# Kernel tuning notes

Hardware: AMD Instinct MI355X
Metric: run time of the kernel (lower is better)

The kernel has to match this reference:

```python
import jax, jax.numpy as jnp
import numpy as np

H, DH = 8, 64            # heads, dim_head (inner_dim = 512)
W_DOT = 1.0              # mask_cond['para']['w_dot']
TOTAL_STEP = 50


def split_heads(x):
    # 'b n (h d) -> (b h) n d'
    b, n, _ = x.shape
    return x.reshape(b, n, H, DH).transpose(0, 2, 1, 3).reshape(b * H, n, DH)


def merge_heads(x):
    # '(b h) n d -> b n (h d)'
    bh, n, d = x.shape
    b = bh // H
    return x.reshape(b, H, n, d).transpose(0, 2, 1, 3).reshape(b, n, H * d)


def setup_inputs() -> dict:
    key = jax.random.key(0)
    ks = jax.random.split(key, 10)
    B, N, DQ, DC, L, C = 1, 4096, 320, 768, 77, 4
    INNER = H * DH
    w = lambda i, shape: jax.random.normal(ks[i], shape, jnp.float32) * 0.02
    return {
        "x": jax.random.normal(ks[0], (2 * B, N, DQ), jnp.float32),
        "uc_context": jax.random.normal(ks[1], (B, L, DC), jnp.float32),
        "ck": jax.random.normal(ks[2], (C, B, L, DC), jnp.float32),
        "cv": jax.random.normal(ks[3], (C, B, L, DC), jnp.float32),
        "attn_extra": jax.random.uniform(ks[4], (H, N, L), jnp.float32),
        "Wq": w(5, (DQ, INNER)),
        "Wk": w(6, (DC, INNER)),
        "Wv": w(7, (DC, INNER)),
        "Wo": w(8, (INNER, DQ)),
        "bo": jnp.zeros((DQ,), jnp.float32),
        "t": 10,
    }


def reference(x, uc_context, ck, cv, attn_extra, Wq, Wk, Wv, Wo, bo, t):
    scale = DH ** (-0.5)
    # schedule()['linear'][TOTAL_STEP - t - 1] == t / 50 * 4.6
    weight = (t / TOTAL_STEP) * 4.6

    B = uc_context.shape[0]
    true_bs = B * H

    q = split_heads(x @ Wq)                          # [(2B)H, N, d]
    k_uc = split_heads(uc_context @ Wk)              # [BH, L, d]
    v_uc = split_heads(uc_context @ Wv)
    k_c = jax.vmap(lambda c: split_heads(c @ Wk))(ck)  # [C, BH, L, d]
    v_c = jax.vmap(lambda c: split_heads(c @ Wv))(cv)

    q_uc, q_c = q[:true_bs], q[true_bs:]
    sim_uc = jnp.einsum('bid,bjd->bij', q_uc, k_uc) * scale     # [BH, N, L]
    sim_c = jnp.einsum('bid,cbjd->cbij', q_c, k_c) * scale      # [C, BH, N, L]

    # region-dependent additive soft mask on the first conditional branch,
    # weighted by w_dot * schedule_weight * max(sim_c[0])
    wmask = W_DOT * weight * sim_c[0].max()
    sim_c = sim_c.at[0].add(wmask * attn_extra)     # attn_extra [H, N, L] broadcasts (B=1)

    attn_uc = jax.nn.softmax(sim_uc, axis=-1)
    attn_c = jax.nn.softmax(sim_c, axis=-1)

    out_uc = jnp.einsum('bij,bjd->bid', attn_uc, v_uc)
    out_c = jnp.einsum('cbij,cbjd->bid', attn_c, v_c) / v_c.shape[0]

    out = jnp.concatenate([out_uc, out_c], axis=0)  # [2BH, N, d]
    out = merge_heads(out)                          # [2B, N, inner]
    return out @ Wo + bo                            # to_out (dropout=0 -> identity)
```

## Files before the change

kernel.cpp:

```cpp
#include <hip/hip_runtime.h>


typedef __attribute__((ext_vector_type(8))) short          bf16x8;
typedef __attribute__((ext_vector_type(4))) float          f32x4;
typedef __attribute__((ext_vector_type(8))) unsigned short u16x8;

#define OFF_XB   0ull
#define OFF_CTXB 5242880ull
#define OFF_WQT  6307840ull
#define OFF_WKT  6635520ull
#define OFF_WVT  7421952ull
#define OFF_WOT  8208384ull
#define OFF_Q    8536064ull
#define OFF_K    16924672ull
#define OFF_VT   17318912ull
#define OFF_ATT  18138112ull
#define OFF_MAX  26526720ull

__device__ __forceinline__ unsigned short bf_cvt(float f) {
  unsigned u = __float_as_uint(f);
  unsigned r = u + 0x7FFFu + ((u >> 16) & 1u);
  return (unsigned short)(r >> 16);
}
__device__ __forceinline__ unsigned enc_f(float f) {
  int b = __float_as_int(f);
  return (b >= 0) ? ((unsigned)b | 0x80000000u) : ~(unsigned)b;
}
__device__ __forceinline__ float dec_f(unsigned u) {
  unsigned b = (u & 0x80000000u) ? (u ^ 0x80000000u) : ~u;
  return __int_as_float((int)b);
}

__global__ __launch_bounds__(256) void k_convert(const float* __restrict__ x,
                                                 const float* __restrict__ uc,
                                                 const float* __restrict__ ck,
                                                 const float* __restrict__ cv,
                                                 unsigned short* __restrict__ xb,
                                                 unsigned short* __restrict__ ctxb,
                                                 unsigned* __restrict__ maxslot) {
  size_t idx = (size_t)blockIdx.x * 256 + threadIdx.x;
  if (idx == 0) *maxslot = 0u;
  if (idx < 655360) {
    float4 v = reinterpret_cast<const float4*>(x)[idx];
    ushort4 o = {bf_cvt(v.x), bf_cvt(v.y), bf_cvt(v.z), bf_cvt(v.w)};
    reinterpret_cast<ushort4*>(xb)[idx] = o;
  } else {
    size_t r = idx - 655360;
    if (r < 133056) {
      const float4* s = (r < 14784) ? (reinterpret_cast<const float4*>(uc) + r)
                      : (r < 73920) ? (reinterpret_cast<const float4*>(ck) + (r - 14784))
                                    : (reinterpret_cast<const float4*>(cv) + (r - 73920));
      float4 v = *s;
      ushort4 o = {bf_cvt(v.x), bf_cvt(v.y), bf_cvt(v.z), bf_cvt(v.w)};
      reinterpret_cast<ushort4*>(ctxb)[r] = o;
    }
  }
}

__global__ __launch_bounds__(256) void k_tw(const float* __restrict__ Wq, const float* __restrict__ Wk,
                                            const float* __restrict__ Wv, const float* __restrict__ Wo,
                                            unsigned short* __restrict__ WqT, unsigned short* __restrict__ WkT,
                                            unsigned short* __restrict__ WvT, unsigned short* __restrict__ WoT) {
  __shared__ float T[32][33];
  int z = blockIdx.z;
  const float* src; unsigned short* dst; int R, C;
  if (z == 0)      { src = Wq; dst = WqT; R = 320; C = 512; }
  else if (z == 1) { src = Wk; dst = WkT; R = 768; C = 512; }
  else if (z == 2) { src = Wv; dst = WvT; R = 768; C = 512; }
  else             { src = Wo; dst = WoT; R = 512; C = 320; }
  int c0 = blockIdx.x * 32, r0 = blockIdx.y * 32;
  if (c0 >= C || r0 >= R) return;
  int t = threadIdx.x;
  {
    int r = t >> 3, c4 = (t & 7) * 4;
    float4 v = *reinterpret_cast<const float4*>(src + (size_t)(r0 + r) * C + c0 + c4);
    T[r][c4] = v.x; T[r][c4 + 1] = v.y; T[r][c4 + 2] = v.z; T[r][c4 + 3] = v.w;
  }
  __syncthreads();
  {
    int c = t >> 3, r4 = (t & 7) * 4;
    ushort4 o = {bf_cvt(T[r4][c]), bf_cvt(T[r4 + 1][c]), bf_cvt(T[r4 + 2][c]), bf_cvt(T[r4 + 3][c])};
    *reinterpret_cast<ushort4*>(dst + (size_t)(c0 + c) * R + r0 + r4) = o;
  }
}

__global__ __launch_bounds__(256) void k_gemm_q(const unsigned short* __restrict__ xb,
                                                const unsigned short* __restrict__ WqT,
                                                unsigned short* __restrict__ q) {
  __shared__ unsigned short As[128 * 40];
  __shared__ unsigned short Bs[128 * 40];
  int tid = threadIdx.x, lane = tid & 63, w = tid >> 6;
  int wr = w >> 1, wc = w & 1, l15 = lane & 15, qd = lane >> 4;
  int mb = blockIdx.x * 128, nb = blockIdx.y * 128;
  f32x4 acc[4][4] = {};
  for (int k0 = 0; k0 < 320; k0 += 32) {
    for (int u = tid; u < 512; u += 256) {
      int r = u >> 2, c8 = (u & 3) * 8;
      *reinterpret_cast<u16x8*>(&As[r * 40 + c8]) =
          *reinterpret_cast<const u16x8*>(&xb[(size_t)(mb + r) * 320 + k0 + c8]);
    }
    for (int u = tid; u < 512; u += 256) {
      int r = u >> 2, c8 = (u & 3) * 8;
      *reinterpret_cast<u16x8*>(&Bs[r * 40 + c8]) =
          *reinterpret_cast<const u16x8*>(&WqT[(size_t)(nb + r) * 320 + k0 + c8]);
    }
    __syncthreads();
    bf16x8 a[4], b[4];
#pragma unroll
    for (int mi = 0; mi < 4; ++mi)
      a[mi] = *reinterpret_cast<const bf16x8*>(&As[(wr * 64 + mi * 16 + l15) * 40 + qd * 8]);
#pragma unroll
    for (int ni = 0; ni < 4; ++ni)
      b[ni] = *reinterpret_cast<const bf16x8*>(&Bs[(wc * 64 + ni * 16 + l15) * 40 + qd * 8]);
#pragma unroll
    for (int mi = 0; mi < 4; ++mi)
#pragma unroll
      for (int ni = 0; ni < 4; ++ni)
        acc[mi][ni] = __builtin_amdgcn_mfma_f32_16x16x32_bf16(a[mi], b[ni], acc[mi][ni], 0, 0, 0);
    __syncthreads();
  }
#pragma unroll
  for (int mi = 0; mi < 4; ++mi)
#pragma unroll
    for (int ni = 0; ni < 4; ++ni)
#pragma unroll
      for (int r = 0; r < 4; ++r) {
        int m = mb + wr * 64 + mi * 16 + qd * 4 + r;
        int n = nb + wc * 64 + ni * 16 + l15;
        int b_ = m >> 12, i = m & 4095, h = n >> 6, d = n & 63;
        q[((size_t)((b_ * 8 + h) * 4096 + i)) * 64 + d] = bf_cvt(acc[mi][ni][r]);
      }
}

__global__ __launch_bounds__(256) void k_gemm_ctx(const unsigned short* __restrict__ ctxb,
                                                  const unsigned short* __restrict__ WkT,
                                                  const unsigned short* __restrict__ WvT,
                                                  unsigned short* __restrict__ kb,
                                                  unsigned short* __restrict__ vt) {
  __shared__ unsigned short As[80 * 40];
  __shared__ unsigned short Bs[64 * 40];
  int tid = threadIdx.x, lane = tid & 63, w = tid >> 6;
  int l15 = lane & 15, qd = lane >> 4;
  int nb = blockIdx.x * 64;
  int g = blockIdx.y;
  int kv = g >= 5, cidx = g % 5;
  int src = kv ? (cidx == 0 ? 0 : 4 + cidx) : (cidx == 0 ? 0 : cidx);
  const unsigned short* WT = kv ? WvT : WkT;
  f32x4 acc[5] = {};
  for (int k0 = 0; k0 < 768; k0 += 32) {
    for (int u = tid; u < 320; u += 256) {
      int r = u >> 2, c8 = (u & 3) * 8;
      u16x8 v = {0, 0, 0, 0, 0, 0, 0, 0};
      if (r < 77) v = *reinterpret_cast<const u16x8*>(&ctxb[(size_t)(src * 77 + r) * 768 + k0 + c8]);
      *reinterpret_cast<u16x8*>(&As[r * 40 + c8]) = v;
    }
    for (int u = tid; u < 256; u += 256) {
      int r = u >> 2, c8 = (u & 3) * 8;
      *reinterpret_cast<u16x8*>(&Bs[r * 40 + c8]) =
          *reinterpret_cast<const u16x8*>(&WT[(size_t)(nb + r) * 768 + k0 + c8]);
    }
    __syncthreads();
    bf16x8 b = *reinterpret_cast<const bf16x8*>(&Bs[(w * 16 + l15) * 40 + qd * 8]);
#pragma unroll
    for (int mi = 0; mi < 5; ++mi) {
      bf16x8 a = *reinterpret_cast<const bf16x8*>(&As[(mi * 16 + l15) * 40 + qd * 8]);
      acc[mi] = __builtin_amdgcn_mfma_f32_16x16x32_bf16(a, b, acc[mi], 0, 0, 0);
    }
    __syncthreads();
  }
#pragma unroll
  for (int mi = 0; mi < 5; ++mi)
#pragma unroll
    for (int r = 0; r < 4; ++r) {
      int j = mi * 16 + qd * 4 + r;
      if (j >= 77) continue;
      int n = nb + w * 16 + l15;
      int h = n >> 6, d = n & 63;
      unsigned short val = bf_cvt(acc[mi][r]);
      if (!kv) kb[((size_t)(cidx * 8 + h) * 77 + j) * 64 + d] = val;
      else     vt[((size_t)(cidx * 8 + h) * 64 + d) * 80 + j] = val;
    }
}

__global__ __launch_bounds__(256) void k_max(const unsigned short* __restrict__ q,
                                             const unsigned short* __restrict__ kb,
                                             unsigned* __restrict__ maxslot) {
  __shared__ unsigned short Ks[80 * 72];
  __shared__ float red[4];
  int tid = threadIdx.x, lane = tid & 63, w = tid >> 6;
  int l15 = lane & 15, qd = lane >> 4;
  int rowbase = blockIdx.x * 128, h = blockIdx.y;
  size_t kbase = (size_t)(1 * 8 + h) * 77 * 64;
  for (int u = tid; u < 640; u += 256) {
    int r = u >> 3, c8 = (u & 7) * 8;
    u16x8 v = {0, 0, 0, 0, 0, 0, 0, 0};
    if (r < 77) v = *reinterpret_cast<const u16x8*>(&kb[kbase + (size_t)r * 64 + c8]);
    *reinterpret_cast<u16x8*>(&Ks[r * 72 + c8]) = v;
  }
  __syncthreads();
  bf16x8 aq[2][2];
#pragma unroll
  for (int mi = 0; mi < 2; ++mi)
#pragma unroll
    for (int ks = 0; ks < 2; ++ks) {
      int row = rowbase + w * 32 + mi * 16 + l15;
      aq[mi][ks] = *reinterpret_cast<const bf16x8*>(&q[((size_t)(8 + h) * 4096 + row) * 64 + qd * 8 + ks * 32]);
    }
  f32x4 acc[2][5] = {};
#pragma unroll
  for (int jf = 0; jf < 5; ++jf)
#pragma unroll
    for (int ks = 0; ks < 2; ++ks) {
      bf16x8 b = *reinterpret_cast<const bf16x8*>(&Ks[(jf * 16 + l15) * 72 + qd * 8 + ks * 32]);
#pragma unroll
      for (int mi = 0; mi < 2; ++mi)
        acc[mi][jf] = __builtin_amdgcn_mfma_f32_16x16x32_bf16(aq[mi][ks], b, acc[mi][jf], 0, 0, 0);
    }
  float lmax = -3.4e38f;
#pragma unroll
  for (int jf = 0; jf < 5; ++jf) {
    int j = jf * 16 + l15;
    if (j < 77) {
#pragma unroll
      for (int mi = 0; mi < 2; ++mi)
#pragma unroll
        for (int r = 0; r < 4; ++r) lmax = fmaxf(lmax, acc[mi][jf][r] * 0.125f);
    }
  }
  for (int m = 1; m < 64; m <<= 1) lmax = fmaxf(lmax, __shfl_xor(lmax, m, 64));
  if (lane == 0) red[w] = lmax;
  __syncthreads();
  if (tid == 0) {
    float m4 = fmaxf(fmaxf(red[0], red[1]), fmaxf(red[2], red[3]));
    atomicMax(maxslot, enc_f(m4));
  }
}

__global__ __launch_bounds__(256) void k_attn(const unsigned short* __restrict__ q,
                                              const unsigned short* __restrict__ kb,
                                              const unsigned short* __restrict__ vt,
                                              const float* __restrict__ extra,
                                              const int* __restrict__ tptr,
                                              const unsigned* __restrict__ maxslot,
                                              unsigned short* __restrict__ att) {
  __shared__ unsigned short Ks[80 * 72];
  __shared__ unsigned short VT[64 * 104];
  __shared__ unsigned short Ps[64 * 104];
  int tid = threadIdx.x, lane = tid & 63, w = tid >> 6;
  int l15 = lane & 15, qd = lane >> 4;
  int rowbase = blockIdx.x * 64, h = blockIdx.y, part = blockIdx.z;
  int bh = part ? 8 + h : h;
  for (int u = tid; u < 1024; u += 256) {
    int d = u >> 4, j = 80 + (u & 15);
    VT[d * 104 + j] = 0;
    Ps[d * 104 + j] = 0;
  }
  int myrow = rowbase + w * 16 + l15;
  bf16x8 aq[2];
  aq[0] = *reinterpret_cast<const bf16x8*>(&q[((size_t)bh * 4096 + myrow) * 64 + qd * 8]);
  aq[1] = *reinterpret_cast<const bf16x8*>(&q[((size_t)bh * 4096 + myrow) * 64 + qd * 8 + 32]);
  float weight = ((float)(*tptr)) * (4.6f / 50.0f);
  float wmask = weight * dec_f(*maxslot);
  int grow = rowbase + w * 16 + qd * 4;
  f32x4 oacc[4] = {};
  int nctx = part ? 4 : 1;
  for (int ci = 0; ci < nctx; ++ci) {
    int slot = part ? 1 + ci : 0;
    __syncthreads();
    size_t kbase = (size_t)(slot * 8 + h) * 77 * 64;
    size_t vbase = (size_t)(slot * 8 + h) * 64 * 80;
    for (int u = tid; u < 640; u += 256) {
      int r = u >> 3, c8 = (u & 7) * 8;
      u16x8 v = {0, 0, 0, 0, 0, 0, 0, 0};
      if (r < 77) v = *reinterpret_cast<const u16x8*>(&kb[kbase + (size_t)r * 64 + c8]);
      *reinterpret_cast<u16x8*>(&Ks[r * 72 + c8]) = v;
    }
    for (int u = tid; u < 640; u += 256) {
      int d = u / 10, c8 = (u % 10) * 8;
      *reinterpret_cast<u16x8*>(&VT[d * 104 + c8]) =
          *reinterpret_cast<const u16x8*>(&vt[vbase + (size_t)d * 80 + c8]);
    }
    __syncthreads();
    f32x4 sim[5];
#pragma unroll
    for (int jf = 0; jf < 5; ++jf) {
      bf16x8 b0 = *reinterpret_cast<const bf16x8*>(&Ks[(jf * 16 + l15) * 72 + qd * 8]);
      bf16x8 b1 = *reinterpret_cast<const bf16x8*>(&Ks[(jf * 16 + l15) * 72 + qd * 8 + 32]);
      f32x4 s = {};
      s = __builtin_amdgcn_mfma_f32_16x16x32_bf16(aq[0], b0, s, 0, 0, 0);
      s = __builtin_amdgcn_mfma_f32_16x16x32_bf16(aq[1], b1, s, 0, 0, 0);
      sim[jf] = s;
    }
    bool isc0 = (part == 1) && (ci == 0);
    float rowsum[4] = {0.f, 0.f, 0.f, 0.f};
    float e[5][4];
#pragma unroll
    for (int jf = 0; jf < 5; ++jf) {
      int j = jf * 16 + l15;
#pragma unroll
      for (int r = 0; r < 4; ++r) {
        float val = sim[jf][r] * 0.125f;
        float ev = 0.f;
        if (j < 77) {
          if (isc0) val += wmask * extra[((size_t)h * 4096 + grow + r) * 77 + j];
          ev = __expf(val);
        }
        e[jf][r] = ev;
        rowsum[r] += ev;
      }
    }
#pragma unroll
    for (int r = 0; r < 4; ++r) {
      float s = rowsum[r];
      s += __shfl_xor(s, 1, 64); s += __shfl_xor(s, 2, 64);
      s += __shfl_xor(s, 4, 64); s += __shfl_xor(s, 8, 64);
      rowsum[r] = s;
    }
#pragma unroll
    for (int jf = 0; jf < 5; ++jf) {
      int j = jf * 16 + l15;
#pragma unroll
      for (int r = 0; r < 4; ++r) Ps[(w * 16 + qd * 4 + r) * 104 + j] = bf_cvt(e[jf][r]);
    }
    bf16x8 pa[3];
#pragma unroll
    for (int ks = 0; ks < 3; ++ks)
      pa[ks] = *reinterpret_cast<const bf16x8*>(&Ps[(w * 16 + l15) * 104 + qd * 8 + ks * 32]);
#pragma unroll
    for (int nf = 0; nf < 4; ++nf) {
      f32x4 o = {};
#pragma unroll
      for (int ks = 0; ks < 3; ++ks) {
        bf16x8 bv = *reinterpret_cast<const bf16x8*>(&VT[(nf * 16 + l15) * 104 + qd * 8 + ks * 32]);
        o = __builtin_amdgcn_mfma_f32_16x16x32_bf16(pa[ks], bv, o, 0, 0, 0);
      }
      if (part == 0) {
#pragma unroll
        for (int r = 0; r < 4; ++r)
          att[((size_t)(grow + r)) * 512 + h * 64 + nf * 16 + l15] = bf_cvt(o[r] / rowsum[r]);
      } else {
#pragma unroll
        for (int r = 0; r < 4; ++r) oacc[nf][r] += o[r] / rowsum[r];
      }
    }
  }
  if (part == 1) {
#pragma unroll
    for (int nf = 0; nf < 4; ++nf)
#pragma unroll
      for (int r = 0; r < 4; ++r)
        att[((size_t)(4096 + grow + r)) * 512 + h * 64 + nf * 16 + l15] = bf_cvt(oacc[nf][r] * 0.25f);
  }
}

__global__ __launch_bounds__(256) void k_gemm_out(const unsigned short* __restrict__ att,
                                                  const unsigned short* __restrict__ WoT,
                                                  const float* __restrict__ bo,
                                                  float* __restrict__ out) {
  __shared__ unsigned short As[128 * 40];
  __shared__ unsigned short Bs[64 * 40];
  int tid = threadIdx.x, lane = tid & 63, w = tid >> 6;
  int l15 = lane & 15, qd = lane >> 4;
  int mb = blockIdx.x * 128, nb = blockIdx.y * 64;
  f32x4 acc[2][4] = {};
  for (int k0 = 0; k0 < 512; k0 += 32) {
    for (int u = tid; u < 512; u += 256) {
      int r = u >> 2, c8 = (u & 3) * 8;
      *reinterpret_cast<u16x8*>(&As[r * 40 + c8]) =
          *reinterpret_cast<const u16x8*>(&att[(size_t)(mb + r) * 512 + k0 + c8]);
    }
    for (int u = tid; u < 256; u += 256) {
      int r = u >> 2, c8 = (u & 3) * 8;
      *reinterpret_cast<u16x8*>(&Bs[r * 40 + c8]) =
          *reinterpret_cast<const u16x8*>(&WoT[(size_t)(nb + r) * 512 + k0 + c8]);
    }
    __syncthreads();
    bf16x8 a[2], b[4];
#pragma unroll
    for (int mi = 0; mi < 2; ++mi)
      a[mi] = *reinterpret_cast<const bf16x8*>(&As[(w * 32 + mi * 16 + l15) * 40 + qd * 8]);
#pragma unroll
    for (int nf = 0; nf < 4; ++nf)
      b[nf] = *reinterpret_cast<const bf16x8*>(&Bs[(nf * 16 + l15) * 40 + qd * 8]);
#pragma unroll
    for (int mi = 0; mi < 2; ++mi)
#pragma unroll
      for (int nf = 0; nf < 4; ++nf)
        acc[mi][nf] = __builtin_amdgcn_mfma_f32_16x16x32_bf16(a[mi], b[nf], acc[mi][nf], 0, 0, 0);
    __syncthreads();
  }
#pragma unroll
  for (int mi = 0; mi < 2; ++mi)
#pragma unroll
    for (int nf = 0; nf < 4; ++nf) {
      int n = nb + nf * 16 + l15;
      float bias = bo[n];
#pragma unroll
      for (int r = 0; r < 4; ++r) {
        int m = mb + w * 32 + mi * 16 + qd * 4 + r;
        out[(size_t)m * 320 + n] = acc[mi][nf][r] + bias;
      }
    }
}

extern "C" void kernel_launch(void* const* d_in, const int* in_sizes, int n_in,
                              void* d_out, int out_size, void* d_ws, size_t ws_size,
                              hipStream_t stream) {
  (void)in_sizes; (void)n_in; (void)out_size; (void)ws_size;
  const float* x  = (const float*)d_in[0];
  const float* uc = (const float*)d_in[1];
  const float* ck = (const float*)d_in[2];
  const float* cv = (const float*)d_in[3];
  const float* ex = (const float*)d_in[4];
  const float* Wq = (const float*)d_in[5];
  const float* Wk = (const float*)d_in[6];
  const float* Wv = (const float*)d_in[7];
  const float* Wo = (const float*)d_in[8];
  const float* bo = (const float*)d_in[9];
  const int*   tp = (const int*)d_in[10];

  char* base = (char*)d_ws;
  unsigned short* xb   = (unsigned short*)(base + OFF_XB);
  unsigned short* ctxb = (unsigned short*)(base + OFF_CTXB);
  unsigned short* WqT  = (unsigned short*)(base + OFF_WQT);
  unsigned short* WkT  = (unsigned short*)(base + OFF_WKT);
  unsigned short* WvT  = (unsigned short*)(base + OFF_WVT);
  unsigned short* WoT  = (unsigned short*)(base + OFF_WOT);
  unsigned short* qb   = (unsigned short*)(base + OFF_Q);
  unsigned short* kb   = (unsigned short*)(base + OFF_K);
  unsigned short* vt   = (unsigned short*)(base + OFF_VT);
  unsigned short* att  = (unsigned short*)(base + OFF_ATT);
  unsigned* maxslot    = (unsigned*)(base + OFF_MAX);

  k_convert<<<3080, 256, 0, stream>>>(x, uc, ck, cv, xb, ctxb, maxslot);
  k_tw<<<dim3(16, 24, 4), 256, 0, stream>>>(Wq, Wk, Wv, Wo, WqT, WkT, WvT, WoT);
  k_gemm_q<<<dim3(64, 4), 256, 0, stream>>>(xb, WqT, qb);
  k_gemm_ctx<<<dim3(8, 10), 256, 0, stream>>>(ctxb, WkT, WvT, kb, vt);
  k_max<<<dim3(32, 8), 256, 0, stream>>>(qb, kb, maxslot);
  k_attn<<<dim3(64, 8, 2), 256, 0, stream>>>(qb, kb, vt, ex, tp, maxslot, att);
  k_gemm_out<<<dim3(64, 5), 256, 0, stream>>>(att, WoT, bo, (float*)d_out);
}
```

Measured before the change: 176.8 us.

## Merge all stages into one persistent cooperative kernel with grid-wide syncs

Replaces the seven separate launches with a single persistent kernel that walks through phases (conversion/transpose, projections, max, attention, output GEMM) and separates them with grid-wide synchronisation. A multi-launch fallback is kept. The per-context attention outputs are now written to separate buffers and averaged while the output GEMM loads its A tile. The Wo tile is loaded with direct global-to-LDS loads and an XOR swizzle. The aim is to remove launch overhead and inter-kernel gaps, at the cost of grid-sync latency, a fixed tile schedule and extra memory traffic for the per-context buffers.

```diff
diff --git a/kernel.cpp b/kernel.cpp
--- a/kernel.cpp
+++ b/kernel.cpp
@@ -1,27 +1,44 @@
 #include <hip/hip_runtime.h>
+#include <hip/hip_cooperative_groups.h>
+
+namespace cg = cooperative_groups;
 
 
 typedef __attribute__((ext_vector_type(8))) short          bf16x8;
 typedef __attribute__((ext_vector_type(4))) float          f32x4;
 typedef __attribute__((ext_vector_type(8))) unsigned short u16x8;
 
-#define OFF_XB   0ull
-#define OFF_CTXB 5242880ull
-#define OFF_WQT  6307840ull
-#define OFF_WKT  6635520ull
-#define OFF_WVT  7421952ull
-#define OFF_WOT  8208384ull
-#define OFF_Q    8536064ull
-#define OFF_K    16924672ull
-#define OFF_VT   17318912ull
-#define OFF_ATT  18138112ull
-#define OFF_MAX  26526720ull
+#define OFF_XB    0ull
+#define OFF_CTXB  5242880ull
+#define OFF_WQT   6307328ull
+#define OFF_WKT   6635008ull
+#define OFF_WVT   7421440ull
+#define OFF_WOT   8207872ull
+#define OFF_QB    8535552ull
+#define OFF_KB    16924160ull
+#define OFF_VTB   17333760ull
+#define OFF_ATT0  18152960ull
+#define OFF_ATTC  22347264ull
+#define OFF_MAX   39124480ull
+
+#define SMEM_BYTES 38400
+
+struct Params {
+  const float *x, *uc, *ck, *cv, *ex, *Wq, *Wk, *Wv, *Wo, *bo;
+  const int* tp;
+  unsigned short *xb, *ctxb, *WqT, *WkT, *WvT, *WoT, *qb, *kb, *vtb, *att0, *attc;
+  unsigned* maxslot;
+  float* out;
+};
 
 __device__ __forceinline__ unsigned short bf_cvt(float f) {
   unsigned u = __float_as_uint(f);
   unsigned r = u + 0x7FFFu + ((u >> 16) & 1u);
   return (unsigned short)(r >> 16);
 }
+__device__ __forceinline__ float bf2f(unsigned short u) {
+  return __uint_as_float(((unsigned)u) << 16);
+}
 __device__ __forceinline__ unsigned enc_f(float f) {
   int b = __float_as_int(f);
   return (b >= 0) ? ((unsigned)b | 0x80000000u) : ~(unsigned)b;
@@ -30,413 +47,406 @@
   unsigned b = (u & 0x80000000u) ? (u ^ 0x80000000u) : ~u;
   return __int_as_float((int)b);
 }
-
-__global__ __launch_bounds__(256) void k_convert(const float* __restrict__ x,
-                                                 const float* __restrict__ uc,
-                                                 const float* __restrict__ ck,
-                                                 const float* __restrict__ cv,
-                                                 unsigned short* __restrict__ xb,
-                                                 unsigned short* __restrict__ ctxb,
-                                                 unsigned* __restrict__ maxslot) {
-  size_t idx = (size_t)blockIdx.x * 256 + threadIdx.x;
-  if (idx == 0) *maxslot = 0u;
-  if (idx < 655360) {
-    float4 v = reinterpret_cast<const float4*>(x)[idx];
-    ushort4 o = {bf_cvt(v.x), bf_cvt(v.y), bf_cvt(v.z), bf_cvt(v.w)};
-    reinterpret_cast<ushort4*>(xb)[idx] = o;
-  } else {
-    size_t r = idx - 655360;
-    if (r < 133056) {
-      const float4* s = (r < 14784) ? (reinterpret_cast<const float4*>(uc) + r)
-                      : (r < 73920) ? (reinterpret_cast<const float4*>(ck) + (r - 14784))
-                                    : (reinterpret_cast<const float4*>(cv) + (r - 73920));
-      float4 v = *s;
-      ushort4 o = {bf_cvt(v.x), bf_cvt(v.y), bf_cvt(v.z), bf_cvt(v.w)};
-      reinterpret_cast<ushort4*>(ctxb)[r] = o;
-    }
-  }
-}
-
-__global__ __launch_bounds__(256) void k_tw(const float* __restrict__ Wq, const float* __restrict__ Wk,
-                                            const float* __restrict__ Wv, const float* __restrict__ Wo,
-                                            unsigned short* __restrict__ WqT, unsigned short* __restrict__ WkT,
-                                            unsigned short* __restrict__ WvT, unsigned short* __restrict__ WoT) {
-  __shared__ float T[32][33];
-  int z = blockIdx.z;
-  const float* src; unsigned short* dst; int R, C;
-  if (z == 0)      { src = Wq; dst = WqT; R = 320; C = 512; }
-  else if (z == 1) { src = Wk; dst = WkT; R = 768; C = 512; }
-  else if (z == 2) { src = Wv; dst = WvT; R = 768; C = 512; }
-  else             { src = Wo; dst = WoT; R = 512; C = 320; }
-  int c0 = blockIdx.x * 32, r0 = blockIdx.y * 32;
-  if (c0 >= C || r0 >= R) return;
-  int t = threadIdx.x;
-  {
-    int r = t >> 3, c4 = (t & 7) * 4;
-    float4 v = *reinterpret_cast<const float4*>(src + (size_t)(r0 + r) * C + c0 + c4);
-    T[r][c4] = v.x; T[r][c4 + 1] = v.y; T[r][c4 + 2] = v.z; T[r][c4 + 3] = v.w;
-  }
-  __syncthreads();
-  {
-    int c = t >> 3, r4 = (t & 7) * 4;
-    ushort4 o = {bf_cvt(T[r4][c]), bf_cvt(T[r4 + 1][c]), bf_cvt(T[r4 + 2][c]), bf_cvt(T[r4 + 3][c])};
-    *reinterpret_cast<ushort4*>(dst + (size_t)(c0 + c) * R + r0 + r4) = o;
-  }
-}
-
-__global__ __launch_bounds__(256) void k_gemm_q(const unsigned short* __restrict__ xb,
-                                                const unsigned short* __restrict__ WqT,
-                                                unsigned short* __restrict__ q) {
-  __shared__ unsigned short As[128 * 40];
-  __shared__ unsigned short Bs[128 * 40];
-  int tid = threadIdx.x, lane = tid & 63, w = tid >> 6;
-  int wr = w >> 1, wc = w & 1, l15 = lane & 15, qd = lane >> 4;
-  int mb = blockIdx.x * 128, nb = blockIdx.y * 128;
-  f32x4 acc[4][4] = {};
-  for (int k0 = 0; k0 < 320; k0 += 32) {
-    for (int u = tid; u < 512; u += 256) {
-      int r = u >> 2, c8 = (u & 3) * 8;
-      *reinterpret_cast<u16x8*>(&As[r * 40 + c8]) =
-          *reinterpret_cast<const u16x8*>(&xb[(size_t)(mb + r) * 320 + k0 + c8]);
-    }
-    for (int u = tid; u < 512; u += 256) {
-      int r = u >> 2, c8 = (u & 3) * 8;
-      *reinterpret_cast<u16x8*>(&Bs[r * 40 + c8]) =
-          *reinterpret_cast<const u16x8*>(&WqT[(size_t)(nb + r) * 320 + k0 + c8]);
-    }
-    __syncthreads();
-    bf16x8 a[4], b[4];
-#pragma unroll
-    for (int mi = 0; mi < 4; ++mi)
-      a[mi] = *reinterpret_cast<const bf16x8*>(&As[(wr * 64 + mi * 16 + l15) * 40 + qd * 8]);
-#pragma unroll
-    for (int ni = 0; ni < 4; ++ni)
-      b[ni] = *reinterpret_cast<const bf16x8*>(&Bs[(wc * 64 + ni * 16 + l15) * 40 + qd * 8]);
-#pragma unroll
-    for (int mi = 0; mi < 4; ++mi)
-#pragma unroll
-      for (int ni = 0; ni < 4; ++ni)
-        acc[mi][ni] = __builtin_amdgcn_mfma_f32_16x16x32_bf16(a[mi], b[ni], acc[mi][ni], 0, 0, 0);
-    __syncthreads();
-  }
-#pragma unroll
-  for (int mi = 0; mi < 4; ++mi)
-#pragma unroll
-    for (int ni = 0; ni < 4; ++ni)
-#pragma unroll
-      for (int r = 0; r < 4; ++r) {
-        int m = mb + wr * 64 + mi * 16 + qd * 4 + r;
-        int n = nb + wc * 64 + ni * 16 + l15;
-        int b_ = m >> 12, i = m & 4095, h = n >> 6, d = n & 63;
-        q[((size_t)((b_ * 8 + h) * 4096 + i)) * 64 + d] = bf_cvt(acc[mi][ni][r]);
-      }
-}
-
-__global__ __launch_bounds__(256) void k_gemm_ctx(const unsigned short* __restrict__ ctxb,
-                                                  const unsigned short* __restrict__ WkT,
-                                                  const unsigned short* __restrict__ WvT,
-                                                  unsigned short* __restrict__ kb,
-                                                  unsigned short* __restrict__ vt) {
-  __shared__ unsigned short As[80 * 40];
-  __shared__ unsigned short Bs[64 * 40];
-  int tid = threadIdx.x, lane = tid & 63, w = tid >> 6;
-  int l15 = lane & 15, qd = lane >> 4;
-  int nb = blockIdx.x * 64;
-  int g = blockIdx.y;
-  int kv = g >= 5, cidx = g % 5;
-  int src = kv ? (cidx == 0 ? 0 : 4 + cidx) : (cidx == 0 ? 0 : cidx);
-  const unsigned short* WT = kv ? WvT : WkT;
-  f32x4 acc[5] = {};
-  for (int k0 = 0; k0 < 768; k0 += 32) {
-    for (int u = tid; u < 320; u += 256) {
-      int r = u >> 2, c8 = (u & 3) * 8;
-      u16x8 v = {0, 0, 0, 0, 0, 0, 0, 0};
-      if (r < 77) v = *reinterpret_cast<const u16x8*>(&ctxb[(size_t)(src * 77 + r) * 768 + k0 + c8]);
-      *reinterpret_cast<u16x8*>(&As[r * 40 + c8]) = v;
-    }
-    for (int u = tid; u < 256; u += 256) {
-      int r = u >> 2, c8 = (u & 3) * 8;
-      *reinterpret_cast<u16x8*>(&Bs[r * 40 + c8]) =
-          *reinterpret_cast<const u16x8*>(&WT[(size_t)(nb + r) * 768 + k0 + c8]);
-    }
-    __syncthreads();
-    bf16x8 b = *reinterpret_cast<const bf16x8*>(&Bs[(w * 16 + l15) * 40 + qd * 8]);
-#pragma unroll
-    for (int mi = 0; mi < 5; ++mi) {
-      bf16x8 a = *reinterpret_cast<const bf16x8*>(&As[(mi * 16 + l15) * 40 + qd * 8]);
-      acc[mi] = __builtin_amdgcn_mfma_f32_16x16x32_bf16(a, b, acc[mi], 0, 0, 0);
-    }
-    __syncthreads();
-  }
-#pragma unroll
-  for (int mi = 0; mi < 5; ++mi)
-#pragma unroll
-    for (int r = 0; r < 4; ++r) {
-      int j = mi * 16 + qd * 4 + r;
-      if (j >= 77) continue;
-      int n = nb + w * 16 + l15;
-      int h = n >> 6, d = n & 63;
-      unsigned short val = bf_cvt(acc[mi][r]);
-      if (!kv) kb[((size_t)(cidx * 8 + h) * 77 + j) * 64 + d] = val;
-      else     vt[((size_t)(cidx * 8 + h) * 64 + d) * 80 + j] = val;
-    }
-}
-
-__global__ __launch_bounds__(256) void k_max(const unsigned short* __restrict__ q,
-                                             const unsigned short* __restrict__ kb,
-                                             unsigned* __restrict__ maxslot) {
-  __shared__ unsigned short Ks[80 * 72];
-  __shared__ float red[4];
-  int tid = threadIdx.x, lane = tid & 63, w = tid >> 6;
-  int l15 = lane & 15, qd = lane >> 4;
-  int rowbase = blockIdx.x * 128, h = blockIdx.y;
-  size_t kbase = (size_t)(1 * 8 + h) * 77 * 64;
-  for (int u = tid; u < 640; u += 256) {
-    int r = u >> 3, c8 = (u & 7) * 8;
-    u16x8 v = {0, 0, 0, 0, 0, 0, 0, 0};
-    if (r < 77) v = *reinterpret_cast<const u16x8*>(&kb[kbase + (size_t)r * 64 + c8]);
-    *reinterpret_cast<u16x8*>(&Ks[r * 72 + c8]) = v;
-  }
-  __syncthreads();
-  bf16x8 aq[2][2];
-#pragma unroll
-  for (int mi = 0; mi < 2; ++mi)
-#pragma unroll
-    for (int ks = 0; ks < 2; ++ks) {
-      int row = rowbase + w * 32 + mi * 16 + l15;
-      aq[mi][ks] = *reinterpret_cast<const bf16x8*>(&q[((size_t)(8 + h) * 4096 + row) * 64 + qd * 8 + ks * 32]);
-    }
-  f32x4 acc[2][5] = {};
-#pragma unroll
-  for (int jf = 0; jf < 5; ++jf)
-#pragma unroll
-    for (int ks = 0; ks < 2; ++ks) {
-      bf16x8 b = *reinterpret_cast<const bf16x8*>(&Ks[(jf * 16 + l15) * 72 + qd * 8 + ks * 32]);
-#pragma unroll
-      for (int mi = 0; mi < 2; ++mi)
-        acc[mi][jf] = __builtin_amdgcn_mfma_f32_16x16x32_bf16(aq[mi][ks], b, acc[mi][jf], 0, 0, 0);
-    }
-  float lmax = -3.4e38f;
-#pragma unroll
-  for (int jf = 0; jf < 5; ++jf) {
-    int j = jf * 16 + l15;
-    if (j < 77) {
-#pragma unroll
-      for (int mi = 0; mi < 2; ++mi)
-#pragma unroll
-        for (int r = 0; r < 4; ++r) lmax = fmaxf(lmax, acc[mi][jf][r] * 0.125f);
-    }
-  }
-  for (int m = 1; m < 64; m <<= 1) lmax = fmaxf(lmax, __shfl_xor(lmax, m, 64));
-  if (lane == 0) red[w] = lmax;
-  __syncthreads();
-  if (tid == 0) {
-    float m4 = fmaxf(fmaxf(red[0], red[1]), fmaxf(red[2], red[3]));
-    atomicMax(maxslot, enc_f(m4));
-  }
-}
-
-__global__ __launch_bounds__(256) void k_attn(const unsigned short* __restrict__ q,
-                                              const unsigned short* __restrict__ kb,
-                                              const unsigned short* __restrict__ vt,
-                                              const float* __restrict__ extra,
-                                              const int* __restrict__ tptr,
-                                              const unsigned* __restrict__ maxslot,
-                                              unsigned short* __restrict__ att) {
-  __shared__ unsigned short Ks[80 * 72];
-  __shared__ unsigned short VT[64 * 104];
-  __shared__ unsigned short Ps[64 * 104];
-  int tid = threadIdx.x, lane = tid & 63, w = tid >> 6;
-  int l15 = lane & 15, qd = lane >> 4;
-  int rowbase = blockIdx.x * 64, h = blockIdx.y, part = blockIdx.z;
-  int bh = part ? 8 + h : h;
-  for (int u = tid; u < 1024; u += 256) {
-    int d = u >> 4, j = 80 + (u & 15);
-    VT[d * 104 + j] = 0;
-    Ps[d * 104 + j] = 0;
-  }
-  int myrow = rowbase + w * 16 + l15;
-  bf16x8 aq[2];
-  aq[0] = *reinterpret_cast<const bf16x8*>(&q[((size_t)bh * 4096 + myrow) * 64 + qd * 8]);
-  aq[1] = *reinterpret_cast<const bf16x8*>(&q[((size_t)bh * 4096 + myrow) * 64 + qd * 8 + 32]);
-  float weight = ((float)(*tptr)) * (4.6f / 50.0f);
-  float wmask = weight * dec_f(*maxslot);
-  int grow = rowbase + w * 16 + qd * 4;
-  f32x4 oacc[4] = {};
-  int nctx = part ? 4 : 1;
-  for (int ci = 0; ci < nctx; ++ci) {
-    int slot = part ? 1 + ci : 0;
-    __syncthreads();
-    size_t kbase = (size_t)(slot * 8 + h) * 77 * 64;
-    size_t vbase = (size_t)(slot * 8 + h) * 64 * 80;
-    for (int u = tid; u < 640; u += 256) {
-      int r = u >> 3, c8 = (u & 7) * 8;
-      u16x8 v = {0, 0, 0, 0, 0, 0, 0, 0};
-      if (r < 77) v = *reinterpret_cast<const u16x8*>(&kb[kbase + (size_t)r * 64 + c8]);
-      *reinterpret_cast<u16x8*>(&Ks[r * 72 + c8]) = v;
-    }
-    for (int u = tid; u < 640; u += 256) {
-      int d = u / 10, c8 = (u % 10) * 8;
-      *reinterpret_cast<u16x8*>(&VT[d * 104 + c8]) =
-          *reinterpret_cast<const u16x8*>(&vt[vbase + (size_t)d * 80 + c8]);
-    }
-    __syncthreads();
-    f32x4 sim[5];
-#pragma unroll
-    for (int jf = 0; jf < 5; ++jf) {
-      bf16x8 b0 = *reinterpret_cast<const bf16x8*>(&Ks[(jf * 16 + l15) * 72 + qd * 8]);
-      bf16x8 b1 = *reinterpret_cast<const bf16x8*>(&Ks[(jf * 16 + l15) * 72 + qd * 8 + 32]);
-      f32x4 s = {};
-      s = __builtin_amdgcn_mfma_f32_16x16x32_bf16(aq[0], b0, s, 0, 0, 0);
-      s = __builtin_amdgcn_mfma_f32_16x16x32_bf16(aq[1], b1, s, 0, 0, 0);
-      sim[jf] = s;
-    }
-    bool isc0 = (part == 1) && (ci == 0);
-    float rowsum[4] = {0.f, 0.f, 0.f, 0.f};
-    float e[5][4];
-#pragma unroll
-    for (int jf = 0; jf < 5; ++jf) {
-      int j = jf * 16 + l15;
-#pragma unroll
-      for (int r = 0; r < 4; ++r) {
-        float val = sim[jf][r] * 0.125f;
-        float ev = 0.f;
-        if (j < 77) {
-          if (isc0) val += wmask * extra[((size_t)h * 4096 + grow + r) * 77 + j];
-          ev = __expf(val);
-        }
-        e[jf][r] = ev;
-        rowsum[r] += ev;
+__device__ __forceinline__ f32x4 mfma16(bf16x8 a, bf16x8 b, f32x4 c) {
+  return __builtin_amdgcn_mfma_f32_16x16x32_bf16(a, b, c, 0, 0, 0);
+}
+__device__ __forceinline__ void gload16(const void* g, void* l) {
+  __builtin_amdgcn_global_load_lds((const __attribute__((address_space(1))) void*)g,
+                                   (__attribute__((address_space(3))) void*)l, 16, 0, 0);
+}
+
+__global__ void __launch_bounds__(256, 4) k_all(Params p, int plo, int phi) {
+  __shared__ __align__(16) char smem[SMEM_BYTES];
+  const int tid  = threadIdx.x;
+  const int lane = tid & 63, w = tid >> 6;
+  const int l15  = lane & 15, qd = lane >> 4;
+
+  for (int ph = plo; ph < phi; ++ph) {
+    if (ph > plo) cg::this_grid().sync();
+
+    if (ph == 0) {
+      const int NVT = 4168;
+      for (int v = blockIdx.x; v < NVT; v += gridDim.x) {
+        if (v < 2560) {
+          size_t idx = (size_t)v * 256 + tid;
+          float4 t = reinterpret_cast<const float4*>(p.x)[idx];
+          ushort4 o = {bf_cvt(t.x), bf_cvt(t.y), bf_cvt(t.z), bf_cvt(t.w)};
+          reinterpret_cast<ushort4*>(p.xb)[idx] = o;
+          if (v == 0 && tid == 0) *p.maxslot = 0u;
+        } else if (v < 3080) {
+          size_t r = (size_t)(v - 2560) * 256 + tid;
+          if (r < 133056) {
+            const float4* s = (r < 14784) ? (reinterpret_cast<const float4*>(p.uc) + r)
+                            : (r < 73920) ? (reinterpret_cast<const float4*>(p.ck) + (r - 14784))
+                                          : (reinterpret_cast<const float4*>(p.cv) + (r - 73920));
+            float4 t = *s;
+            ushort4 o = {bf_cvt(t.x), bf_cvt(t.y), bf_cvt(t.z), bf_cvt(t.w)};
+            reinterpret_cast<ushort4*>(p.ctxb)[r] = o;
+          }
+        } else {
+          int q = v - 3080;
+          const float* src; unsigned short* dst; int R, C, rt, ct;
+          if (q < 160)      { src = p.Wq; dst = p.WqT; R = 320; C = 512; rt = q / 16; ct = q % 16; }
+          else if (q < 544) { q -= 160; src = p.Wk; dst = p.WkT; R = 768; C = 512; rt = q / 16; ct = q % 16; }
+          else if (q < 928) { q -= 544; src = p.Wv; dst = p.WvT; R = 768; C = 512; rt = q / 16; ct = q % 16; }
+          else              { q -= 928; src = p.Wo; dst = p.WoT; R = 512; C = 320; rt = q / 10; ct = q % 10; }
+          float* T = reinterpret_cast<float*>(smem);
+          int r0 = rt * 32, c0 = ct * 32;
+          __syncthreads();
+          { int r = tid >> 3, c4 = (tid & 7) * 4;
+            float4 t = *reinterpret_cast<const float4*>(src + (size_t)(r0 + r) * C + c0 + c4);
+            T[r * 33 + c4] = t.x; T[r * 33 + c4 + 1] = t.y;
+            T[r * 33 + c4 + 2] = t.z; T[r * 33 + c4 + 3] = t.w; }
+          __syncthreads();
+          { int c = tid >> 3, r4 = (tid & 7) * 4;
+            ushort4 o = {bf_cvt(T[r4 * 33 + c]), bf_cvt(T[(r4 + 1) * 33 + c]),
+                         bf_cvt(T[(r4 + 2) * 33 + c]), bf_cvt(T[(r4 + 3) * 33 + c])};
+            *reinterpret_cast<ushort4*>(dst + (size_t)(c0 + c) * R + r0 + r4) = o; }
+        }
       }
     }
-#pragma unroll
-    for (int r = 0; r < 4; ++r) {
-      float s = rowsum[r];
-      s += __shfl_xor(s, 1, 64); s += __shfl_xor(s, 2, 64);
-      s += __shfl_xor(s, 4, 64); s += __shfl_xor(s, 8, 64);
-      rowsum[r] = s;
+
+    else if (ph == 1) {
+      const int NVT = 592;
+      for (int v = blockIdx.x; v < NVT; v += gridDim.x) {
+        __syncthreads();
+        if (v < 512) {
+          int mb = (v >> 3) * 128, nb = (v & 7) * 64;
+          unsigned short* As = reinterpret_cast<unsigned short*>(smem);
+          unsigned short* Bs = reinterpret_cast<unsigned short*>(smem + 8192);
+          int wr = w >> 1, wc = w & 1;
+          f32x4 acc[4][2] = {};
+          for (int k0 = 0; k0 < 320; k0 += 32) {
+#pragma unroll
+            for (int ii = 0; ii < 2; ++ii) {
+              int i = w * 2 + ii;
+              int r = i * 16 + (lane >> 2), cs = lane & 3;
+              gload16(p.xb + (size_t)(mb + r) * 320 + k0 + ((cs ^ (r & 3)) * 8), As + i * 512);
+            }
+            { int r = w * 16 + (lane >> 2), cs = lane & 3;
+              gload16(p.WqT + (size_t)(nb + r) * 320 + k0 + ((cs ^ (r & 3)) * 8), Bs + w * 512); }
+            __syncthreads();
+            bf16x8 a[4], b[2];
+#pragma unroll
+            for (int mi = 0; mi < 4; ++mi) {
+              int row = wr * 64 + mi * 16 + l15;
+              a[mi] = *reinterpret_cast<const bf16x8*>(&As[row * 32 + ((qd ^ (row & 3)) * 8)]);
+            }
+#pragma unroll
+            for (int ni = 0; ni < 2; ++ni) {
+              int row = wc * 32 + ni * 16 + l15;
+              b[ni] = *reinterpret_cast<const bf16x8*>(&Bs[row * 32 + ((qd ^ (row & 3)) * 8)]);
+            }
+#pragma unroll
+            for (int mi = 0; mi < 4; ++mi)
+#pragma unroll
+              for (int ni = 0; ni < 2; ++ni)
+                acc[mi][ni] = mfma16(a[mi], b[ni], acc[mi][ni]);
+            __syncthreads();
+          }
+#pragma unroll
+          for (int mi = 0; mi < 4; ++mi)
+#pragma unroll
+            for (int ni = 0; ni < 2; ++ni)
+#pragma unroll
+              for (int r = 0; r < 4; ++r) {
+                int m = mb + wr * 64 + mi * 16 + qd * 4 + r;
+                int n = nb + wc * 32 + ni * 16 + l15;
+                int b_ = m >> 12, i = m & 4095, h = n >> 6, d = n & 63;
+                p.qb[((size_t)((b_ * 8 + h) * 4096 + i)) * 64 + d] = bf_cvt(acc[mi][ni][r]);
+              }
+        } else {
+          int u2 = v - 512;
+          int g = u2 >> 3, nb = (u2 & 7) * 64;
+          int kv = g >= 5, cidx = g % 5;
+          int s77 = kv ? (cidx == 0 ? 0 : 4 + cidx) : (cidx == 0 ? 0 : cidx);
+          const unsigned short* WT = kv ? p.WvT : p.WkT;
+          unsigned short* Ac = reinterpret_cast<unsigned short*>(smem);
+          unsigned short* Bc = reinterpret_cast<unsigned short*>(smem + 10240);
+          f32x4 acc[5] = {};
+          for (int k0 = 0; k0 < 768; k0 += 64) {
+#pragma unroll
+            for (int t = 0; t < 3; ++t) {
+              int i = w + t * 4;
+              if (i < 10) {
+                int r = i * 8 + (lane >> 3), cs = lane & 7;
+                gload16(p.ctxb + (size_t)(s77 * 77 + r) * 768 + k0 + ((cs ^ (r & 7)) * 8),
+                        Ac + i * 512);
+              }
+            }
+#pragma unroll
+            for (int t = 0; t < 2; ++t) {
+              int i = w * 2 + t;
+              int r = i * 8 + (lane >> 3), cs = lane & 7;
+              gload16(WT + (size_t)(nb + r) * 768 + k0 + ((cs ^ (r & 7)) * 8), Bc + i * 512);
+            }
+            __syncthreads();
+#pragma unroll
+            for (int ks = 0; ks < 2; ++ks) {
+              int rb = w * 16 + l15;
+              bf16x8 b = *reinterpret_cast<const bf16x8*>(&Bc[rb * 64 + (((ks * 4 + qd) ^ (rb & 7)) * 8)]);
+#pragma unroll
+              for (int mi = 0; mi < 5; ++mi) {
+                int ra = mi * 16 + l15;
+                bf16x8 a = *reinterpret_cast<const bf16x8*>(&Ac[ra * 64 + (((ks * 4 + qd) ^ (ra & 7)) * 8)]);
+                acc[mi] = mfma16(a, b, acc[mi]);
+              }
+            }
+            __syncthreads();
+          }
+#pragma unroll
+          for (int mi = 0; mi < 5; ++mi)
+#pragma unroll
+            for (int r = 0; r < 4; ++r) {
+              int j = mi * 16 + qd * 4 + r;
+              int n = nb + w * 16 + l15, h = n >> 6, d = n & 63;
+              unsigned short val = (j < 77) ? bf_cvt(acc[mi][r]) : (unsigned short)0;
+              if (kv) p.vtb[((size_t)(cidx * 8 + h) * 64 + d) * 80 + j] = val;
+              else    p.kb[((size_t)(cidx * 8 + h) * 80 + j) * 64 + d] = val;
+            }
+        }
+      }
     }
-#pragma unroll
-    for (int jf = 0; jf < 5; ++jf) {
-      int j = jf * 16 + l15;
-#pragma unroll
-      for (int r = 0; r < 4; ++r) Ps[(w * 16 + qd * 4 + r) * 104 + j] = bf_cvt(e[jf][r]);
+
+    else if (ph == 2) {
+      const int NVT = 512;
+      for (int v = blockIdx.x; v < NVT; v += gridDim.x) {
+        __syncthreads();
+        int rt = v >> 3, h = v & 7;
+        int rowbase = rt * 64;
+        unsigned short* Ks = reinterpret_cast<unsigned short*>(smem);
+        size_t kbase = (size_t)(1 * 8 + h) * 80 * 64;
+        for (int u = tid; u < 640; u += 256) {
+          int r = u >> 3, c8 = (u & 7) * 8;
+          *reinterpret_cast<u16x8*>(&Ks[r * 72 + c8]) =
+              *reinterpret_cast<const u16x8*>(&p.kb[kbase + (size_t)r * 64 + c8]);
+        }
+        __syncthreads();
+        int myrow = rowbase + w * 16 + l15;
+        bf16x8 aq0 = *reinterpret_cast<const bf16x8*>(&p.qb[((size_t)(8 + h) * 4096 + myrow) * 64 + qd * 8]);
+        bf16x8 aq1 = *reinterpret_cast<const bf16x8*>(&p.qb[((size_t)(8 + h) * 4096 + myrow) * 64 + qd * 8 + 32]);
+        float lmax = -3.4e38f;
+#pragma unroll
+        for (int jf = 0; jf < 5; ++jf) {
+          bf16x8 b0 = *reinterpret_cast<const bf16x8*>(&Ks[(jf * 16 + l15) * 72 + qd * 8]);
+          bf16x8 b1 = *reinterpret_cast<const bf16x8*>(&Ks[(jf * 16 + l15) * 72 + qd * 8 + 32]);
+          f32x4 s = {};
+          s = mfma16(aq0, b0, s);
+          s = mfma16(aq1, b1, s);
+          if (jf * 16 + l15 < 77) {
+#pragma unroll
+            for (int r = 0; r < 4; ++r) lmax = fmaxf(lmax, s[r] * 0.125f);
+          }
+        }
+        for (int m = 1; m < 64; m <<= 1) lmax = fmaxf(lmax, __shfl_xor(lmax, m, 64));
+        float* red = reinterpret_cast<float*>(smem + 11776);
+        if (lane == 0) red[w] = lmax;
+        __syncthreads();
+        if (tid == 0)
+          atomicMax(p.maxslot, enc_f(fmaxf(fmaxf(red[0], red[1]), fmaxf(red[2], red[3]))));
+      }
     }
-    bf16x8 pa[3];
-#pragma unroll
-    for (int ks = 0; ks < 3; ++ks)
-      pa[ks] = *reinterpret_cast<const bf16x8*>(&Ps[(w * 16 + l15) * 104 + qd * 8 + ks * 32]);
-#pragma unroll
-    for (int nf = 0; nf < 4; ++nf) {
-      f32x4 o = {};
-#pragma unroll
-      for (int ks = 0; ks < 3; ++ks) {
-        bf16x8 bv = *reinterpret_cast<const bf16x8*>(&VT[(nf * 16 + l15) * 104 + qd * 8 + ks * 32]);
-        o = __builtin_amdgcn_mfma_f32_16x16x32_bf16(pa[ks], bv, o, 0, 0, 0);
+
+    else if (ph == 3) {
+      const int NVT = 2560;
+      const float weight = ((float)(*p.tp)) * (4.6f / 50.0f);
+      for (int v = blockIdx.x; v < NVT; v += gridDim.x) {
+        __syncthreads();
+        int rt = v / 40, rem = v % 40;
+        int h = rem / 5, slot = rem % 5;
+        int rowbase = rt * 64;
+        int bh = slot ? 8 + h : h;
+        unsigned short* Ks = reinterpret_cast<unsigned short*>(smem);
+        unsigned short* VT = reinterpret_cast<unsigned short*>(smem + 11520);
+        unsigned short* Ps = reinterpret_cast<unsigned short*>(smem + 24832);
+        for (int u = tid; u < 1024; u += 256) {
+          int d = u >> 4, j = 80 + (u & 15);
+          VT[d * 104 + j] = 0; Ps[d * 104 + j] = 0;
+        }
+        size_t kbase = (size_t)(slot * 8 + h) * 80 * 64;
+        size_t vbase = (size_t)(slot * 8 + h) * 64 * 80;
+        for (int u = tid; u < 640; u += 256) {
+          int r = u >> 3, c8 = (u & 7) * 8;
+          *reinterpret_cast<u16x8*>(&Ks[r * 72 + c8]) =
+              *reinterpret_cast<const u16x8*>(&p.kb[kbase + (size_t)r * 64 + c8]);
+        }
+        for (int u = tid; u < 640; u += 256) {
+          int d = u / 10, c8 = (u % 10) * 8;
+          *reinterpret_cast<u16x8*>(&VT[d * 104 + c8]) =
+              *reinterpret_cast<const u16x8*>(&p.vtb[vbase + (size_t)d * 80 + c8]);
+        }
+        int myrow = rowbase + w * 16 + l15;
+        bf16x8 aq0 = *reinterpret_cast<const bf16x8*>(&p.qb[((size_t)bh * 4096 + myrow) * 64 + qd * 8]);
+        bf16x8 aq1 = *reinterpret_cast<const bf16x8*>(&p.qb[((size_t)bh * 4096 + myrow) * 64 + qd * 8 + 32]);
+        __syncthreads();
+        f32x4 sim[5];
+#pragma unroll
+        for (int jf = 0; jf < 5; ++jf) {
+          bf16x8 b0 = *reinterpret_cast<const bf16x8*>(&Ks[(jf * 16 + l15) * 72 + qd * 8]);
+          bf16x8 b1 = *reinterpret_cast<const bf16x8*>(&Ks[(jf * 16 + l15) * 72 + qd * 8 + 32]);
+          f32x4 s = {};
+          s = mfma16(aq0, b0, s);
+          s = mfma16(aq1, b1, s);
+          sim[jf] = s;
+        }
+        float wmask_ = (slot == 1) ? weight * dec_f(*p.maxslot) : 0.f;
+        int grow = rowbase + w * 16 + qd * 4;
+        float rowsum[4] = {0.f, 0.f, 0.f, 0.f};
+        float e[5][4];
+#pragma unroll
+        for (int jf = 0; jf < 5; ++jf) {
+          int j = jf * 16 + l15;
+#pragma unroll
+          for (int r = 0; r < 4; ++r) {
+            float ev = 0.f;
+            if (j < 77) {
+              float val = sim[jf][r] * 0.125f;
+              if (slot == 1) val += wmask_ * p.ex[((size_t)h * 4096 + grow + r) * 77 + j];
+              ev = __expf(val);
+            }
+            e[jf][r] = ev;
+            rowsum[r] += ev;
+          }
+        }
+#pragma unroll
+        for (int r = 0; r < 4; ++r) {
+          float s = rowsum[r];
+          s += __shfl_xor(s, 1, 64); s += __shfl_xor(s, 2, 64);
+          s += __shfl_xor(s, 4, 64); s += __shfl_xor(s, 8, 64);
+          rowsum[r] = 1.0f / s;
+        }
+#pragma unroll
+        for (int jf = 0; jf < 5; ++jf) {
+          int j = jf * 16 + l15;
+#pragma unroll
+          for (int r = 0; r < 4; ++r)
+            Ps[(w * 16 + qd * 4 + r) * 104 + j] = bf_cvt(e[jf][r] * rowsum[r]);
+        }
+        bf16x8 pa[3];
+#pragma unroll
+        for (int ks = 0; ks < 3; ++ks)
+          pa[ks] = *reinterpret_cast<const bf16x8*>(&Ps[(w * 16 + l15) * 104 + qd * 8 + ks * 32]);
+#pragma unroll
+        for (int nf = 0; nf < 4; ++nf) {
+          f32x4 o = {};
+#pragma unroll
+          for (int ks = 0; ks < 3; ++ks) {
+            bf16x8 bv = *reinterpret_cast<const bf16x8*>(&VT[(nf * 16 + l15) * 104 + qd * 8 + ks * 32]);
+            o = mfma16(pa[ks], bv, o);
+          }
+          if (slot == 0) {
+#pragma unroll
+            for (int r = 0; r < 4; ++r)
+              p.att0[((size_t)(grow + r)) * 512 + h * 64 + nf * 16 + l15] = bf_cvt(o[r]);
+          } else {
+#pragma unroll
+            for (int r = 0; r < 4; ++r)
+              p.attc[((size_t)((slot - 1) * 4096 + grow + r)) * 512 + h * 64 + nf * 16 + l15] = bf_cvt(o[r]);
+          }
+        }
       }
-      if (part == 0) {
-#pragma unroll
-        for (int r = 0; r < 4; ++r)
-          att[((size_t)(grow + r)) * 512 + h * 64 + nf * 16 + l15] = bf_cvt(o[r] / rowsum[r]);
-      } else {
-#pragma unroll
-        for (int r = 0; r < 4; ++r) oacc[nf][r] += o[r] / rowsum[r];
+    }
+
+    else {
+      const int NVT = 640;
+      for (int v = blockIdx.x; v < NVT; v += gridDim.x) {
+        __syncthreads();
+        int mb = (v / 5) * 64, nb = (v % 5) * 64;
+        bool ucpart = (mb < 4096);
+        int mb2 = mb - 4096;
+        unsigned short* As = reinterpret_cast<unsigned short*>(smem);
+        unsigned short* Bs = reinterpret_cast<unsigned short*>(smem + 5120);
+        f32x4 acc[4] = {};
+        for (int k0 = 0; k0 < 512; k0 += 32) {
+          { int r = tid >> 2, cs = tid & 3;
+            u16x8 val;
+            if (ucpart) {
+              val = *reinterpret_cast<const u16x8*>(&p.att0[(size_t)(mb + r) * 512 + k0 + cs * 8]);
+            } else {
+              float f[8] = {0.f, 0.f, 0.f, 0.f, 0.f, 0.f, 0.f, 0.f};
+#pragma unroll
+              for (int ci = 0; ci < 4; ++ci) {
+                u16x8 t = *reinterpret_cast<const u16x8*>(
+                    &p.attc[((size_t)(ci * 4096 + mb2 + r)) * 512 + k0 + cs * 8]);
+#pragma unroll
+                for (int e2 = 0; e2 < 8; ++e2) f[e2] += bf2f((unsigned short)t[e2]);
+              }
+#pragma unroll
+              for (int e2 = 0; e2 < 8; ++e2) val[e2] = bf_cvt(f[e2] * 0.25f);
+            }
+            *reinterpret_cast<u16x8*>(&As[r * 40 + cs * 8]) = val;
+          }
+          { int r = w * 16 + (lane >> 2), cs = lane & 3;
+            gload16(p.WoT + (size_t)(nb + r) * 512 + k0 + ((cs ^ (r & 3)) * 8), Bs + w * 512); }
+          __syncthreads();
+          bf16x8 a = *reinterpret_cast<const bf16x8*>(&As[(w * 16 + l15) * 40 + qd * 8]);
+#pragma unroll
+          for (int nf = 0; nf < 4; ++nf) {
+            int rb = nf * 16 + l15;
+            bf16x8 b = *reinterpret_cast<const bf16x8*>(&Bs[rb * 32 + ((qd ^ (rb & 3)) * 8)]);
+            acc[nf] = mfma16(a, b, acc[nf]);
+          }
+          __syncthreads();
+        }
+#pragma unroll
+        for (int nf = 0; nf < 4; ++nf) {
+          int n = nb + nf * 16 + l15;
+          float bias = p.bo[n];
+#pragma unroll
+          for (int r = 0; r < 4; ++r)
+            p.out[(size_t)(mb + w * 16 + qd * 4 + r) * 320 + n] = acc[nf][r] + bias;
+        }
       }
     }
   }
-  if (part == 1) {
-#pragma unroll
-    for (int nf = 0; nf < 4; ++nf)
-#pragma unroll
-      for (int r = 0; r < 4; ++r)
-        att[((size_t)(4096 + grow + r)) * 512 + h * 64 + nf * 16 + l15] = bf_cvt(oacc[nf][r] * 0.25f);
-  }
-}
-
-__global__ __launch_bounds__(256) void k_gemm_out(const unsigned short* __restrict__ att,
-                                                  const unsigned short* __restrict__ WoT,
-                                                  const float* __restrict__ bo,
-                                                  float* __restrict__ out) {
-  __shared__ unsigned short As[128 * 40];
-  __shared__ unsigned short Bs[64 * 40];
-  int tid = threadIdx.x, lane = tid & 63, w = tid >> 6;
-  int l15 = lane & 15, qd = lane >> 4;
-  int mb = blockIdx.x * 128, nb = blockIdx.y * 64;
-  f32x4 acc[2][4] = {};
-  for (int k0 = 0; k0 < 512; k0 += 32) {
-    for (int u = tid; u < 512; u += 256) {
-      int r = u >> 2, c8 = (u & 3) * 8;
-      *reinterpret_cast<u16x8*>(&As[r * 40 + c8]) =
-          *reinterpret_cast<const u16x8*>(&att[(size_t)(mb + r) * 512 + k0 + c8]);
-    }
-    for (int u = tid; u < 256; u += 256) {
-      int r = u >> 2, c8 = (u & 3) * 8;
-      *reinterpret_cast<u16x8*>(&Bs[r * 40 + c8]) =
-          *reinterpret_cast<const u16x8*>(&WoT[(size_t)(nb + r) * 512 + k0 + c8]);
-    }
-    __syncthreads();
-    bf16x8 a[2], b[4];
-#pragma unroll
-    for (int mi = 0; mi < 2; ++mi)
-      a[mi] = *reinterpret_cast<const bf16x8*>(&As[(w * 32 + mi * 16 + l15) * 40 + qd * 8]);
-#pragma unroll
-    for (int nf = 0; nf < 4; ++nf)
-      b[nf] = *reinterpret_cast<const bf16x8*>(&Bs[(nf * 16 + l15) * 40 + qd * 8]);
-#pragma unroll
-    for (int mi = 0; mi < 2; ++mi)
-#pragma unroll
-      for (int nf = 0; nf < 4; ++nf)
-        acc[mi][nf] = __builtin_amdgcn_mfma_f32_16x16x32_bf16(a[mi], b[nf], acc[mi][nf], 0, 0, 0);
-    __syncthreads();
-  }
-#pragma unroll
-  for (int mi = 0; mi < 2; ++mi)
-#pragma unroll
-    for (int nf = 0; nf < 4; ++nf) {
-      int n = nb + nf * 16 + l15;
-      float bias = bo[n];
-#pragma unroll
-      for (int r = 0; r < 4; ++r) {
-        int m = mb + w * 32 + mi * 16 + qd * 4 + r;
-        out[(size_t)m * 320 + n] = acc[mi][nf][r] + bias;
-      }
-    }
 }
 
 extern "C" void kernel_launch(void* const* d_in, const int* in_sizes, int n_in,
                               void* d_out, int out_size, void* d_ws, size_t ws_size,
                               hipStream_t stream) {
   (void)in_sizes; (void)n_in; (void)out_size; (void)ws_size;
-  const float* x  = (const float*)d_in[0];
-  const float* uc = (const float*)d_in[1];
-  const float* ck = (const float*)d_in[2];
-  const float* cv = (const float*)d_in[3];
-  const float* ex = (const float*)d_in[4];
-  const float* Wq = (const float*)d_in[5];
-  const float* Wk = (const float*)d_in[6];
-  const float* Wv = (const float*)d_in[7];
-  const float* Wo = (const float*)d_in[8];
-  const float* bo = (const float*)d_in[9];
-  const int*   tp = (const int*)d_in[10];
-
   char* base = (char*)d_ws;
-  unsigned short* xb   = (unsigned short*)(base + OFF_XB);
-  unsigned short* ctxb = (unsigned short*)(base + OFF_CTXB);
-  unsigned short* WqT  = (unsigned short*)(base + OFF_WQT);
-  unsigned short* WkT  = (unsigned short*)(base + OFF_WKT);
-  unsigned short* WvT  = (unsigned short*)(base + OFF_WVT);
-  unsigned short* WoT  = (unsigned short*)(base + OFF_WOT);
-  unsigned short* qb   = (unsigned short*)(base + OFF_Q);
-  unsigned short* kb   = (unsigned short*)(base + OFF_K);
-  unsigned short* vt   = (unsigned short*)(base + OFF_VT);
-  unsigned short* att  = (unsigned short*)(base + OFF_ATT);
-  unsigned* maxslot    = (unsigned*)(base + OFF_MAX);
-
-  k_convert<<<3080, 256, 0, stream>>>(x, uc, ck, cv, xb, ctxb, maxslot);
-  k_tw<<<dim3(16, 24, 4), 256, 0, stream>>>(Wq, Wk, Wv, Wo, WqT, WkT, WvT, WoT);
-  k_gemm_q<<<dim3(64, 4), 256, 0, stream>>>(xb, WqT, qb);
-  k_gemm_ctx<<<dim3(8, 10), 256, 0, stream>>>(ctxb, WkT, WvT, kb, vt);
-  k_max<<<dim3(32, 8), 256, 0, stream>>>(qb, kb, maxslot);
-  k_attn<<<dim3(64, 8, 2), 256, 0, stream>>>(qb, kb, vt, ex, tp, maxslot, att);
-  k_gemm_out<<<dim3(64, 5), 256, 0, stream>>>(att, WoT, bo, (float*)d_out);
-}
+  Params p;
+  p.x  = (const float*)d_in[0];
+  p.uc = (const float*)d_in[1];
+  p.ck = (const float*)d_in[2];
+  p.cv = (const float*)d_in[3];
+  p.ex = (const float*)d_in[4];
+  p.Wq = (const float*)d_in[5];
+  p.Wk = (const float*)d_in[6];
+  p.Wv = (const float*)d_in[7];
+  p.Wo = (const float*)d_in[8];
+  p.bo = (const float*)d_in[9];
+  p.tp = (const int*)d_in[10];
+  p.xb   = (unsigned short*)(base + OFF_XB);
+  p.ctxb = (unsigned short*)(base + OFF_CTXB);
+  p.WqT  = (unsigned short*)(base + OFF_WQT);
+  p.WkT  = (unsigned short*)(base + OFF_WKT);
+  p.WvT  = (unsigned short*)(base + OFF_WVT);
+  p.WoT  = (unsigned short*)(base + OFF_WOT);
+  p.qb   = (unsigned short*)(base + OFF_QB);
+  p.kb   = (unsigned short*)(base + OFF_KB);
+  p.vtb  = (unsigned short*)(base + OFF_VTB);
+  p.att0 = (unsigned short*)(base + OFF_ATT0);
+  p.attc = (unsigned short*)(base + OFF_ATTC);
+  p.maxslot = (unsigned*)(base + OFF_MAX);
+  p.out = (float*)d_out;
+
+  int nb = 0;
+  if (hipOccupancyMaxActiveBlocksPerMultiprocessor(&nb, (const void*)k_all, 256, 0) != hipSuccess || nb < 1)
+    nb = 4;
+  int ncu = 256;
+  hipDeviceGetAttribute(&ncu, hipDeviceAttributeMultiprocessorCount, 0);
+  int grid = nb * ncu;
+  if (grid > 2560) grid = 2560;
+  if (grid < 64) grid = 64;
+
+  int plo = 0, phi = 5;
+  void* args[] = {&p, &plo, &phi};
+  hipError_t e = hipLaunchCooperativeKernel((void*)k_all, dim3(grid), dim3(256), args, 0, stream);
+  if (e != hipSuccess) {
+    (void)hipGetLastError();
+    for (int ph = 0; ph < 5; ++ph)
+      k_all<<<grid, 256, 0, stream>>>(p, ph, ph + 1);
+  }
+}
```

New measurement: 430.3 us. 2.43x slower.
